# Optimization experiments

Measured on AMD Instinct MI355X. Metric: run time of the kernel, lower is better.

Reference implementation:

```python
import jax, jax.numpy as jnp
import numpy as np

NB = 50  # nb_steps
IN_D = 64
HID = 128
B = 256


def _cc_weights(nb):
    # Faithful port of UMNN compute_cc_weights (Clenshaw-Curtis quadrature)
    lam = np.arange(0, nb + 1).reshape(-1, 1).astype(np.float64)
    lam = np.cos((lam @ lam.T) * np.pi / nb)
    lam[:, 0] = 0.5
    lam[:, -1] = 0.5 * lam[:, -1]
    lam = lam * 2.0 / nb
    W = np.arange(0, nb + 1).reshape(-1, 1).astype(np.float64)
    W[np.arange(1, nb + 1, 2)] = 0
    W = 2.0 / (1.0 - W ** 2)
    W[0] = 1
    W[np.arange(1, nb + 1, 2)] = 0
    cc = (lam.T @ W)[:, 0].astype(np.float32)              # [nb+1]
    steps = np.cos(np.arange(0, nb + 1) * np.pi / nb).astype(np.float32)  # [nb+1]
    return jnp.asarray(cc), jnp.asarray(steps)


def setup_inputs() -> dict:
    key = jax.random.key(0)
    ks = jax.random.split(key, 16)
    d = {}
    d["x"] = jax.random.normal(ks[0], (B, 1), dtype=jnp.float32)
    d["h"] = jax.random.normal(ks[1], (B, IN_D - 1), dtype=jnp.float32)

    def lin(kw, kb, fan_in, fan_out):
        s = 1.0 / np.sqrt(fan_in)
        w = jax.random.uniform(kw, (fan_in, fan_out), jnp.float32, -s, s)
        b = jax.random.uniform(kb, (fan_out,), jnp.float32, -s, s)
        return w, b

    # Integrand MLP: in_d -> 128 -> 128 -> 1
    d["iw0"], d["ib0"] = lin(ks[2], ks[3], IN_D, HID)
    d["iw1"], d["ib1"] = lin(ks[4], ks[5], HID, HID)
    d["iw2"], d["ib2"] = lin(ks[6], ks[7], HID, 1)
    # Outer net: (in_d-1) -> 128 -> 128 -> 2
    d["nw0"], d["nb0"] = lin(ks[8], ks[9], IN_D - 1, HID)
    d["nw1"], d["nb1"] = lin(ks[10], ks[11], HID, HID)
    d["nw2"], d["nb2"] = lin(ks[12], ks[13], HID, 2)
    return d


def reference(x, h, iw0, ib0, iw1, ib1, iw2, ib2, nw0, nb0, nw1, nb1, nw2, nb2):
    cc, steps = _cc_weights(NB)  # [S1], [S1]
    S1 = NB + 1
    b = x.shape[0]

    # ----- outer quadrature: integral over t in [0, x] -----
    # t[b, i] = 0 + (x - 0) * (steps[i] + 1) / 2
    t = x[:, None, :] * (steps[None, :, None] + 1.0) / 2.0          # [B, S1, 1]

    # ----- inner UMNN: integral over s in [t, xmax], xmax = max(t) + 10 -----
    xmax = jnp.max(t) + 10.0
    s = t[:, :, None, :] + (xmax - t)[:, :, None, :] * (steps[None, None, :, None] + 1.0) / 2.0  # [B,S1,S1,1]

    hb = jnp.broadcast_to(h[:, None, None, :], (b, S1, S1, h.shape[1]))
    inp = jnp.concatenate([s, hb], axis=-1)                         # [B,S1,S1,in_d]

    # PostiveIntegrandNN: Lin-ReLU-Lin-ReLU-Lin-ELU, then + 1.0
    a = jax.nn.relu(inp @ iw0 + ib0)
    a = jax.nn.relu(a @ iw1 + ib1)
    f = jax.nn.elu(a @ iw2 + ib2) + 1.0                              # [B,S1,S1,1]

    # inner Clenshaw-Curtis reduction: z * (xT - x0) / 2
    inner = jnp.sum(f * cc[None, None, :, None], axis=2) * (xmax - t) / 2.0   # [B,S1,1]

    # outer reduction: integral from 0 to x
    outer = jnp.sum(inner * cc[None, :, None], axis=1) * x / 2.0    # [B,1]

    # outer dense net on h -> offset / scaling
    o = jax.nn.relu(h @ nw0 + nb0)
    o = jax.nn.relu(o @ nw1 + nb1)
    o = o @ nw2 + nb2                                               # [B,2]
    offset = o[:, 0:1]
    scaling = jnp.exp(o[:, 1:2])
    return scaling * outer + offset
```

## Files before the change

kernel.cpp:

```cpp
#include <hip/hip_runtime.h>
#include <math.h>

#define NBQ 50
#define S1 51
#define NPTS 2601
#define NTILES 163
#define IN_D 64
#define HID 128
#define BSZ 256
#define NCHUNK 8
#define NUMAX 21

typedef __bf16 bf16x8 __attribute__((ext_vector_type(8)));
typedef float  f32x4  __attribute__((ext_vector_type(4)));

#define WS_CC     0
#define WS_STEPS  64
#define WS_XMAX   128
#define WS_BASE   256
#define WS_SCAL   33024
#define WS_OFF    33280
#define WS_PART   33536
#define WS_W1BF   35840

__global__ void k_prep(const float* __restrict__ x, const float* __restrict__ h,
                       const float* __restrict__ iw0, const float* __restrict__ ib0,
                       const float* __restrict__ iw1,
                       const float* __restrict__ nw0, const float* __restrict__ nb0,
                       const float* __restrict__ nw1, const float* __restrict__ nb1,
                       const float* __restrict__ nw2, const float* __restrict__ nb2,
                       float* __restrict__ ws) {
    int blk = blockIdx.x;
    int tid = threadIdx.x;

    if (blk < 64) {
        int idx  = blk * 256 + tid;
        int e    = idx & 7;
        int lane = (idx >> 3) & 63;
        int fk   = idx >> 9;
        int kk   = fk & 3;
        int nt   = fk >> 2;
        int k = kk * 32 + (lane >> 4) * 8 + e;
        int n = nt * 16 + (lane & 15);
        __bf16* w1bf = (__bf16*)(ws + WS_W1BF);
        w1bf[idx] = (__bf16)iw1[k * HID + n];
        return;
    }

    __shared__ float s_steps[S1];
    __shared__ float s_red[4];
    __shared__ float s_h[IN_D - 1];
    __shared__ float s_o0[HID];
    __shared__ float s_part[4];

    if (blk == 64) {
        int t = tid;
        if (t < S1) {
            double st = cos((double)t * M_PI / (double)NBQ);
            s_steps[t] = (float)st;
            ws[WS_STEPS + t] = (float)st;
            double acc = 0.0;
            for (int i = 0; i <= NBQ; ++i) {
                double Wi;
                if (i == 0)       Wi = 1.0;
                else if (i & 1)   Wi = 0.0;
                else              Wi = 2.0 / (1.0 - (double)i * (double)i);
                double lam;
                if (t == 0)  lam = 0.5;
                else         lam = cos((double)i * (double)t * M_PI / (double)NBQ);
                if (t == NBQ) lam *= 0.5;
                lam *= 2.0 / (double)NBQ;
                acc += lam * Wi;
            }
            ws[WS_CC + t] = (float)acc;
        }
        __syncthreads();
        float xb = x[t];
        float m = -1e30f;
        for (int i = 0; i < S1; ++i)
            m = fmaxf(m, xb * (s_steps[i] + 1.0f) * 0.5f);
        for (int off = 32; off > 0; off >>= 1)
            m = fmaxf(m, __shfl_down(m, off));
        if ((t & 63) == 0) s_red[t >> 6] = m;
        __syncthreads();
        if (t == 0) {
            float mm = fmaxf(fmaxf(s_red[0], s_red[1]), fmaxf(s_red[2], s_red[3]));
            ws[WS_XMAX] = mm + 10.0f;
        }
        return;
    }

    int b = blk - 65;
    int n = tid;
    bool act = (n < HID);
    if (act && n < IN_D - 1) s_h[n] = h[b * (IN_D - 1) + n];
    __syncthreads();
    float o1 = 0.0f;
    if (act) {
        float accB = ib0[n];
        float acc0 = nb0[n];
        for (int d = 0; d < IN_D - 1; ++d) {
            float hv = s_h[d];
            accB = fmaf(hv, iw0[(1 + d) * HID + n], accB);
            acc0 = fmaf(hv, nw0[d * HID + n], acc0);
        }
        ws[WS_BASE + b * HID + n] = accB;
        s_o0[n] = fmaxf(acc0, 0.0f);
    }
    __syncthreads();
    if (act) {
        float acc1 = nb1[n];
        for (int m = 0; m < HID; ++m)
            acc1 = fmaf(s_o0[m], nw1[m * HID + n], acc1);
        o1 = fmaxf(acc1, 0.0f);
    }
    float p0 = act ? o1 * nw2[n * 2 + 0] : 0.0f;
    float p1 = act ? o1 * nw2[n * 2 + 1] : 0.0f;
    for (int off = 32; off > 0; off >>= 1) {
        p0 += __shfl_down(p0, off);
        p1 += __shfl_down(p1, off);
    }
    int lane = tid & 63, w = tid >> 6;
    if (lane == 0 && w < 2) { s_part[w * 2] = p0; s_part[w * 2 + 1] = p1; }
    __syncthreads();
    if (tid == 0) {
        ws[WS_OFF + b]  = s_part[0] + s_part[2] + nb2[0];
        ws[WS_SCAL + b] = expf(s_part[1] + s_part[3] + nb2[1]);
    }
}

__global__ __launch_bounds__(64, 1) void k3_mfma(
        const float* __restrict__ x,
        const float* __restrict__ iw0,
        const float* __restrict__ ib1,
        const float* __restrict__ iw2,
        const float* __restrict__ ib2,
        float* __restrict__ ws) {
    __shared__ float s_cc[S1];
    __shared__ float s_ti[S1];
    __shared__ float s_w[S1];
    __shared__ float s_sjh[S1];
    __shared__ float s_ccw[S1];
    __shared__ float zlds[NUMAX][68];

    int blk  = blockIdx.x;
    int b    = blk >> 3;
    int c    = blk & 7;
    int lane = threadIdx.x;
    int col  = lane & 15;
    int g    = lane >> 4;

    float xmax = ws[WS_XMAX];
    float xb   = x[b];
    float b2   = ib2[0];

    if (lane < S1) {
        float st = ws[WS_STEPS + lane];
        float cc = ws[WS_CC + lane];
        float ti = xb * (st + 1.0f) * 0.5f;
        float w  = xmax - ti;
        s_cc[lane]  = cc;
        s_ti[lane]  = ti;
        s_w[lane]   = w;
        s_sjh[lane] = (st + 1.0f) * 0.5f;
        s_ccw[lane] = cc * w;
    }

    const bf16x8* w1f = (const bf16x8*)(ws + WS_W1BF);
    bf16x8 Af[8][4];
#pragma unroll
    for (int nt = 0; nt < 8; ++nt)
#pragma unroll
        for (int kk = 0; kk < 4; ++kk)
            Af[nt][kk] = w1f[(nt * 4 + kk) * 64 + lane];

    const float* basep = ws + WS_BASE + b * HID;
    f32x4 w0a[4], w0b[4], bsa[4], bsb[4];
#pragma unroll
    for (int kk = 0; kk < 4; ++kk) {
        int m0 = kk * 32 + g * 8;
        w0a[kk] = *(const f32x4*)(iw0 + m0);
        w0b[kk] = *(const f32x4*)(iw0 + m0 + 4);
        bsa[kk] = *(const f32x4*)(basep + m0);
        bsb[kk] = *(const f32x4*)(basep + m0 + 4);
    }

    f32x4 accInit[8], iw2v[8];
#pragma unroll
    for (int nt = 0; nt < 8; ++nt) {
        accInit[nt] = *(const f32x4*)(ib1 + nt * 16 + g * 4);
        iw2v[nt]    = *(const f32x4*)(iw2 + nt * 16 + g * 4);
    }

    __syncthreads();

    int NU = (c <= 2) ? 21 : 20;

    {
    }
    int pc0 = c * 16 + col;
    if (pc0 >= NPTS) pc0 = NPTS - 1;
    int i_c = (int)(((unsigned)pc0 * 10281u) >> 19);
    int j_c = pc0 - i_c * 51;
    float s_cur = fmaf(s_w[i_c], s_sjh[j_c], s_ti[i_c]);

    for (int u = 0; u < NU; ++u) {
        bf16x8 bfr[4];
#pragma unroll
        for (int kk = 0; kk < 4; ++kk) {
#pragma unroll
            for (int e = 0; e < 4; ++e) {
                bfr[kk][e]     = (__bf16)fmaxf(fmaf(s_cur, w0a[kk][e], bsa[kk][e]), 0.0f);
                bfr[kk][4 + e] = (__bf16)fmaxf(fmaf(s_cur, w0b[kk][e], bsb[kk][e]), 0.0f);
            }
        }

        int t2 = c + 8 * (u + 1);
        int pc2 = t2 * 16 + col;
        if (pc2 >= NPTS) pc2 = NPTS - 1;
        int i_n = (int)(((unsigned)pc2 * 10281u) >> 19);
        int j_n = pc2 - i_n * 51;
        float s_nxt = fmaf(s_w[i_n], s_sjh[j_n], s_ti[i_n]);

        f32x4 acc[8];
#pragma unroll
        for (int kk = 0; kk < 4; ++kk)
#pragma unroll
            for (int nt = 0; nt < 8; ++nt)
                acc[nt] = __builtin_amdgcn_mfma_f32_16x16x32_bf16(
                    Af[nt][kk], bfr[kk], (kk == 0) ? accInit[nt] : acc[nt], 0, 0, 0);

        float z0 = 0.f, z1 = 0.f, z2 = 0.f, z3 = 0.f;
#pragma unroll
        for (int nt = 0; nt < 8; ++nt) {
            z0 = fmaf(fmaxf(acc[nt][0], 0.0f), iw2v[nt][0], z0);
            z1 = fmaf(fmaxf(acc[nt][1], 0.0f), iw2v[nt][1], z1);
            z2 = fmaf(fmaxf(acc[nt][2], 0.0f), iw2v[nt][2], z2);
            z3 = fmaf(fmaxf(acc[nt][3], 0.0f), iw2v[nt][3], z3);
        }
        zlds[u][g * 16 + col] = (z0 + z1) + (z2 + z3);

        s_cur = s_nxt;
    }

    float vsum = 0.0f;
    int npass = (NU + 3) >> 2;
    for (int pass = 0; pass < npass; ++pass) {
        int u = pass * 4 + g;
        if (u < NU) {
            int t = c + 8 * u;
            int p = t * 16 + col;
            if (p < NPTS) {
                float z = zlds[u][col] + zlds[u][16 + col]
                        + zlds[u][32 + col] + zlds[u][48 + col] + b2;
                float f = (z > 0.0f) ? (z + 1.0f) : __expf(z);
                int i = (int)(((unsigned)p * 10281u) >> 19);
                int j = p - i * 51;
                vsum += s_ccw[i] * s_cc[j] * f;
            }
        }
    }

#pragma unroll
    for (int off = 1; off < 64; off <<= 1)
        vsum += __shfl_xor(vsum, off);
    if (lane == 0)
        ws[WS_PART + blk] = vsum * 0.5f;
}

__global__ void k4_final(const float* __restrict__ x, const float* __restrict__ ws,
                         float* __restrict__ out) {
    int b = threadIdx.x;
    float sum = 0.0f;
#pragma unroll
    for (int c = 0; c < NCHUNK; ++c) sum += ws[WS_PART + b * NCHUNK + c];
    out[b] = ws[WS_SCAL + b] * sum * x[b] * 0.5f + ws[WS_OFF + b];
}

extern "C" void kernel_launch(void* const* d_in, const int* in_sizes, int n_in,
                              void* d_out, int out_size, void* d_ws, size_t ws_size,
                              hipStream_t stream) {
    const float* x   = (const float*)d_in[0];
    const float* h   = (const float*)d_in[1];
    const float* iw0 = (const float*)d_in[2];
    const float* ib0 = (const float*)d_in[3];
    const float* iw1 = (const float*)d_in[4];
    const float* ib1 = (const float*)d_in[5];
    const float* iw2 = (const float*)d_in[6];
    const float* ib2 = (const float*)d_in[7];
    const float* nw0 = (const float*)d_in[8];
    const float* nb0 = (const float*)d_in[9];
    const float* nw1 = (const float*)d_in[10];
    const float* nb1 = (const float*)d_in[11];
    const float* nw2 = (const float*)d_in[12];
    const float* nb2 = (const float*)d_in[13];
    float* ws  = (float*)d_ws;
    float* out = (float*)d_out;

    hipLaunchKernelGGL(k_prep, dim3(64 + 1 + BSZ), dim3(256), 0, stream,
                       x, h, iw0, ib0, iw1, nw0, nb0, nw1, nb1, nw2, nb2, ws);
    hipLaunchKernelGGL(k3_mfma, dim3(BSZ * NCHUNK), dim3(64), 0, stream,
                       x, iw0, ib1, iw2, ib2, ws);
    hipLaunchKernelGGL(k4_final, dim3(1), dim3(BSZ), 0, stream, x, ws, out);
}
```

Before: 51.16 us.

## Split hidden-layer N tiles across two waves per block in MFMA kernel

Each block now runs two waves, and each wave computes four of the eight 16-column output tiles of the second MLP layer. Partial layer-3 dot products go to per-wave LDS slots and are combined by wave 0 after a barrier. This halves the per-wave register footprint for weight fragments and accumulators and doubles the waves available to hide MFMA latency. The cost is that both waves recompute the first-layer activations, plus an extra block-wide sync and extra LDS reads in the reduction.

```diff
diff --git a/kernel.cpp b/kernel.cpp
--- a/kernel.cpp
+++ b/kernel.cpp
@@ -129,7 +129,7 @@
     }
 }
 
-__global__ __launch_bounds__(64, 1) void k3_mfma(
+__global__ __launch_bounds__(128, 2) void k3_mfma(
         const float* __restrict__ x,
         const float* __restrict__ iw0,
         const float* __restrict__ ib1,
@@ -141,12 +141,14 @@
     __shared__ float s_w[S1];
     __shared__ float s_sjh[S1];
     __shared__ float s_ccw[S1];
-    __shared__ float zlds[NUMAX][68];
+    __shared__ float zlds[2][NUMAX][68];
 
     int blk  = blockIdx.x;
     int b    = blk >> 3;
     int c    = blk & 7;
-    int lane = threadIdx.x;
+    int tid  = threadIdx.x;
+    int wave = tid >> 6;
+    int lane = tid & 63;
     int col  = lane & 15;
     int g    = lane >> 4;
 
@@ -154,25 +156,27 @@
     float xb   = x[b];
     float b2   = ib2[0];
 
-    if (lane < S1) {
-        float st = ws[WS_STEPS + lane];
-        float cc = ws[WS_CC + lane];
+    if (tid < S1) {
+        float st = ws[WS_STEPS + tid];
+        float cc = ws[WS_CC + tid];
         float ti = xb * (st + 1.0f) * 0.5f;
         float w  = xmax - ti;
-        s_cc[lane]  = cc;
-        s_ti[lane]  = ti;
-        s_w[lane]   = w;
-        s_sjh[lane] = (st + 1.0f) * 0.5f;
-        s_ccw[lane] = cc * w;
+        s_cc[tid]  = cc;
+        s_ti[tid]  = ti;
+        s_w[tid]   = w;
+        s_sjh[tid] = (st + 1.0f) * 0.5f;
+        s_ccw[tid] = cc * w;
     }
 
     const bf16x8* w1f = (const bf16x8*)(ws + WS_W1BF);
-    bf16x8 Af[8][4];
-#pragma unroll
-    for (int nt = 0; nt < 8; ++nt)
+    bf16x8 Af[4][4];
+#pragma unroll
+    for (int nt = 0; nt < 4; ++nt) {
+        int NT = wave * 4 + nt;
 #pragma unroll
         for (int kk = 0; kk < 4; ++kk)
-            Af[nt][kk] = w1f[(nt * 4 + kk) * 64 + lane];
+            Af[nt][kk] = w1f[(NT * 4 + kk) * 64 + lane];
+    }
 
     const float* basep = ws + WS_BASE + b * HID;
     f32x4 w0a[4], w0b[4], bsa[4], bsb[4];
@@ -185,19 +189,18 @@
         bsb[kk] = *(const f32x4*)(basep + m0 + 4);
     }
 
-    f32x4 accInit[8], iw2v[8];
-#pragma unroll
-    for (int nt = 0; nt < 8; ++nt) {
-        accInit[nt] = *(const f32x4*)(ib1 + nt * 16 + g * 4);
-        iw2v[nt]    = *(const f32x4*)(iw2 + nt * 16 + g * 4);
+    f32x4 accInit[4], iw2v[4];
+#pragma unroll
+    for (int nt = 0; nt < 4; ++nt) {
+        int n0 = (wave * 4 + nt) * 16 + g * 4;
+        accInit[nt] = *(const f32x4*)(ib1 + n0);
+        iw2v[nt]    = *(const f32x4*)(iw2 + n0);
     }
 
     __syncthreads();
 
     int NU = (c <= 2) ? 21 : 20;
 
-    {
-    }
     int pc0 = c * 16 + col;
     if (pc0 >= NPTS) pc0 = NPTS - 1;
     int i_c = (int)(((unsigned)pc0 * 10281u) >> 19);
@@ -222,50 +225,55 @@
         int j_n = pc2 - i_n * 51;
         float s_nxt = fmaf(s_w[i_n], s_sjh[j_n], s_ti[i_n]);
 
-        f32x4 acc[8];
+        f32x4 acc[4];
 #pragma unroll
         for (int kk = 0; kk < 4; ++kk)
 #pragma unroll
-            for (int nt = 0; nt < 8; ++nt)
+            for (int nt = 0; nt < 4; ++nt)
                 acc[nt] = __builtin_amdgcn_mfma_f32_16x16x32_bf16(
                     Af[nt][kk], bfr[kk], (kk == 0) ? accInit[nt] : acc[nt], 0, 0, 0);
 
         float z0 = 0.f, z1 = 0.f, z2 = 0.f, z3 = 0.f;
 #pragma unroll
-        for (int nt = 0; nt < 8; ++nt) {
+        for (int nt = 0; nt < 4; ++nt) {
             z0 = fmaf(fmaxf(acc[nt][0], 0.0f), iw2v[nt][0], z0);
             z1 = fmaf(fmaxf(acc[nt][1], 0.0f), iw2v[nt][1], z1);
             z2 = fmaf(fmaxf(acc[nt][2], 0.0f), iw2v[nt][2], z2);
             z3 = fmaf(fmaxf(acc[nt][3], 0.0f), iw2v[nt][3], z3);
         }
-        zlds[u][g * 16 + col] = (z0 + z1) + (z2 + z3);
+        zlds[wave][u][g * 16 + col] = (z0 + z1) + (z2 + z3);
 
         s_cur = s_nxt;
     }
 
-    float vsum = 0.0f;
-    int npass = (NU + 3) >> 2;
-    for (int pass = 0; pass < npass; ++pass) {
-        int u = pass * 4 + g;
-        if (u < NU) {
-            int t = c + 8 * u;
-            int p = t * 16 + col;
-            if (p < NPTS) {
-                float z = zlds[u][col] + zlds[u][16 + col]
-                        + zlds[u][32 + col] + zlds[u][48 + col] + b2;
-                float f = (z > 0.0f) ? (z + 1.0f) : __expf(z);
-                int i = (int)(((unsigned)p * 10281u) >> 19);
-                int j = p - i * 51;
-                vsum += s_ccw[i] * s_cc[j] * f;
+    __syncthreads();
+
+    if (wave == 0) {
+        float vsum = 0.0f;
+        int npass = (NU + 3) >> 2;
+        for (int pass = 0; pass < npass; ++pass) {
+            int u = pass * 4 + g;
+            if (u < NU) {
+                int t = c + 8 * u;
+                int p = t * 16 + col;
+                if (p < NPTS) {
+                    float z = zlds[0][u][col] + zlds[0][u][16 + col]
+                            + zlds[0][u][32 + col] + zlds[0][u][48 + col]
+                            + zlds[1][u][col] + zlds[1][u][16 + col]
+                            + zlds[1][u][32 + col] + zlds[1][u][48 + col] + b2;
+                    float f = (z > 0.0f) ? (z + 1.0f) : __expf(z);
+                    int i = (int)(((unsigned)p * 10281u) >> 19);
+                    int j = p - i * 51;
+                    vsum += s_ccw[i] * s_cc[j] * f;
+                }
             }
         }
-    }
-
-#pragma unroll
-    for (int off = 1; off < 64; off <<= 1)
-        vsum += __shfl_xor(vsum, off);
-    if (lane == 0)
-        ws[WS_PART + blk] = vsum * 0.5f;
+#pragma unroll
+        for (int off = 1; off < 64; off <<= 1)
+            vsum += __shfl_xor(vsum, off);
+        if (lane == 0)
+            ws[WS_PART + blk] = vsum * 0.5f;
+    }
 }
 
 __global__ void k4_final(const float* __restrict__ x, const float* __restrict__ ws,
@@ -299,7 +307,7 @@
 
     hipLaunchKernelGGL(k_prep, dim3(64 + 1 + BSZ), dim3(256), 0, stream,
                        x, h, iw0, ib0, iw1, nw0, nb0, nw1, nb1, nw2, nb2, ws);
-    hipLaunchKernelGGL(k3_mfma, dim3(BSZ * NCHUNK), dim3(64), 0, stream,
+    hipLaunchKernelGGL(k3_mfma, dim3(BSZ * NCHUNK), dim3(128), 0, stream,
                        x, iw0, ib1, iw2, ib2, ws);
     hipLaunchKernelGGL(k4_final, dim3(1), dim3(BSZ), 0, stream, x, ws, out);
 }
```

Measured after the change: 51.81 us. No clear change (+1.3%).
